# Performance work log

Hardware: AMD Instinct MI355X
Metric: run time of the kernel (lower is better)

## Reference

```python
import jax, jax.numpy as jnp
import numpy as np
from jax import lax

# ---- quantum-kernel constants: flipped model f = Tr[rho(theta) O(patch)] ----
# rho(theta) = (I + sum_i theta_i P_i)/4 over the 15 non-identity 2-qubit Paulis.
# O(patch)  = (M + M^T)/2 where M is the 3x3 patch zero-padded to 16 and reshaped 4x4.
# Both are linear in their inputs, so precompute A[i,k] = Re Tr[P_i O(e_k)] and
# t0[k] = Tr[O(e_k)] once on the host.

def _pauli_features():
    I = np.eye(2, dtype=np.complex64)
    X = np.array([[0, 1], [1, 0]], np.complex64)
    Y = np.array([[0, -1j], [1j, 0]], np.complex64)
    Z = np.array([[1, 0], [0, -1]], np.complex64)
    singles = [I, X, Y, Z]
    paulis = [np.kron(a, b) for a in singles for b in singles][1:]  # 15 non-identity
    A = np.zeros((15, 9), np.float32)
    t0 = np.zeros((9,), np.float32)
    for k in range(9):
        M = np.zeros((4, 4), np.complex64)
        M.flat[k] = 1.0
        O = (M + M.conj().T) / 2.0
        t0[k] = float(np.real(np.trace(O)))
        for i, P in enumerate(paulis):
            A[i, k] = float(np.real(np.trace(P @ O)))
    return A, t0

_A_NP, _T0_NP = _pauli_features()
STRIDE = 1
PAD = (1, 1)  # (pad_h, pad_w)


def setup_inputs() -> dict:
    key = jax.random.key(0)
    k1, k2, k3 = jax.random.split(key, 3)
    x = jax.random.normal(k1, (32, 16, 128, 128), dtype=jnp.float32)
    weight = jax.random.normal(k2, (64, 16, 15), dtype=jnp.float32)
    bias = jax.random.normal(k3, (64, 1), dtype=jnp.float32)
    return {"x": x, "weight": weight, "bias": bias}


def reference(x, weight, bias):
    B, C, H, W = x.shape
    ph, pw = PAD
    Ho = (H - 3 + 2 * ph) // STRIDE + 1
    Wo = (W - 3 + 2 * pw) // STRIDE + 1
    # im2col: [B, C*9, Ho, Wo], channel-major (C slowest, 3x3 row-major fastest)
    patches = lax.conv_general_dilated_patches(
        x, (3, 3), (STRIDE, STRIDE), ((ph, ph), (pw, pw)))
    patches = patches.reshape(B, C, 9, Ho * Wo)  # [B, C, 9, P]

    A = jnp.asarray(_A_NP)    # [15, 9]
    t0 = jnp.asarray(_T0_NP)  # [9]

    # identity part of rho: sum over in-channels of Tr[O]/4 (weight-independent)
    base = jnp.einsum('k,bckp->bp', t0, patches)            # [B, P]
    # Pauli features Tr[P_i O(patch)] per (channel, patch)
    qf = jnp.einsum('ik,bckp->bcip', A, patches)            # [B, C, 15, P]
    out = (base[:, None, :] + jnp.einsum('oci,bcip->bop', weight, qf)) * 0.25
    out = out + bias                                        # bias [O,1] -> [B,O,P]
    return out.reshape(B, weight.shape[0], Ho, Wo)
```

## Files before the change

kernel.cpp:

```cpp
#include <hip/hip_runtime.h>
#include <hip/hip_bf16.h>


typedef short bf16x8 __attribute__((ext_vector_type(8)));
typedef float f32x4 __attribute__((ext_vector_type(4)));

__device__ __forceinline__ void pauli_entry(int s, int r, int c, float& re, float& im) {
    re = 0.f; im = 0.f;
    if (s == 0)      { if (r == c) re = 1.f; }
    else if (s == 1) { if (r != c) re = 1.f; }
    else if (s == 2) { if (r == 0 && c == 1) im = -1.f; else if (r == 1 && c == 0) im = 1.f; }
    else             { if (r == c) re = (r == 0) ? 1.f : -1.f; }
}

__device__ __forceinline__ float A_entry(int i, int k) {
    int j = i + 1, sa = j >> 2, sb = j & 3;
    int r = k >> 2, c = k & 3;
    float ar, ai, br, bi;
    pauli_entry(sa, r >> 1, c >> 1, ar, ai);
    pauli_entry(sb, r & 1, c & 1, br, bi);
    float re1 = ar * br - ai * bi;
    pauli_entry(sa, c >> 1, r >> 1, ar, ai);
    pauli_entry(sb, c & 1, r & 1, br, bi);
    float re2 = ar * br - ai * bi;
    return 0.5f * (re1 + re2);
}

__device__ __forceinline__ short f2bf(float f) {
    union { float f; unsigned int u; } a; a.f = f;
    unsigned int r = a.u + 0x7fffu + ((a.u >> 16) & 1u);
    return (short)(r >> 16);
}

__device__ __forceinline__ unsigned pk_bf16(float a, float b) {
#if __has_builtin(__builtin_amdgcn_cvt_pk_bf16_f32)
    typedef __bf16 bf2 __attribute__((ext_vector_type(2)));
    bf2 r = __builtin_amdgcn_cvt_pk_bf16_f32(a, b);
    union { bf2 v; unsigned u; } cv; cv.v = r;
    return cv.u;
#else
    union { float f; unsigned u; } x, y; x.f = a; y.f = b;
    unsigned ra = x.u + 0x7fffu + ((x.u >> 16) & 1u);
    unsigned rb = y.u + 0x7fffu + ((y.u >> 16) & 1u);
    return (ra >> 16) | (rb & 0xffff0000u);
#endif
}

__global__ __launch_bounds__(256) void prep_kernel(const float* __restrict__ weight,
                                                   short* __restrict__ bfrag) {
    int t = blockIdx.x * 256 + threadIdx.x;
    if (t >= 1280) return;
    int lane  = t & 63;
    int ot    = (t >> 6) & 3;
    int chunk = t >> 8;
    int q     = lane >> 4;
    int o     = ot * 16 + (lane & 15);
    short vals[8];
    #pragma unroll
    for (int j = 0; j < 8; ++j) {
        int gk = chunk * 32 + q * 8 + j;
        float v = 0.f;
        if (gk < 144) {
            int tap = gk >> 4;
            int c   = gk & 15;
            float acc = (tap == 0 || tap == 5) ? 1.f : 0.f;
            const float* w = weight + (o * 16 + c) * 15;
            #pragma unroll
            for (int i = 0; i < 15; ++i) acc += w[i] * A_entry(i, tap);
            v = 0.25f * acc;
        }
        vals[j] = f2bf(v);
    }
    *(bf16x8*)(bfrag + t * 8) = *(bf16x8*)vals;
}

__global__ __launch_bounds__(256) void conv_mfma(const float* __restrict__ x,
                                                 const short* __restrict__ bfrag,
                                                 const float* __restrict__ bias,
                                                 float* __restrict__ out) {
    __shared__ short sx[10 * 136 * 16];

    const int tid  = threadIdx.x;
    const int h0   = blockIdx.x * 8;
    const int b    = blockIdx.y;
    const int lane = tid & 63;
    const int wave = tid >> 6;
    const int q    = lane >> 4;
    const int nlo  = lane & 15;

    const float* xb = x + (size_t)b * 16 * 128 * 128;
    #pragma unroll
    for (int it = 0; it < 11; ++it) {
        int pos = tid + it * 256;
        if (pos < 2720) {
            int seg = pos / 136;
            int w   = pos - seg * 136;
            int row = seg >> 1, chalf = seg & 1;
            int hp  = h0 - 1 + row;
            int xw  = w - 4;
            bool ok = ((unsigned)hp < 128u) && ((unsigned)xw < 128u);
            const float* src = xb + (size_t)(chalf * 8) * 16384 + hp * 128 + xw;
            float v[8];
            #pragma unroll
            for (int j = 0; j < 8; ++j)
                v[j] = ok ? src[(size_t)j * 16384] : 0.f;
            int slot = (chalf ^ (w >> 2)) & 1;
            unsigned* dst = (unsigned*)sx + (row * 136 + w) * 8 + slot * 4;
            #pragma unroll
            for (int j2 = 0; j2 < 4; ++j2)
                dst[j2] = pk_bf16(v[2 * j2], v[2 * j2 + 1]);
        }
    }

    bf16x8 Breg[20];
    #pragma unroll
    for (int i = 0; i < 20; ++i)
        Breg[i] = *(const bf16x8*)(bfrag + (i * 64 + lane) * 8);
    float bv[4];
    #pragma unroll
    for (int ot = 0; ot < 4; ++ot) bv[ot] = bias[ot * 16 + nlo];

    int baseA[5];
    #pragma unroll
    for (int ch = 0; ch < 5; ++ch) {
        int tap = ch * 2 + (q >> 1);
        if (tap > 8) tap = 8;
        int kh = tap / 3, kw = tap - 3 * kh;
        int chalf = q & 1;
        int row0  = wave * 2 + kh;
        int w0    = nlo + kw + 3;
        int slot  = (chalf ^ (w0 >> 2)) & 1;
        baseA[ch] = (row0 * 136 + w0) * 16 + slot * 8;
    }
    __syncthreads();

    #pragma unroll
    for (int rs = 0; rs < 2; ++rs) {
        const int h = h0 + wave * 2 + rs;
        #pragma unroll
        for (int np = 0; np < 4; ++np) {
            f32x4 acc[2][4];
            #pragma unroll
            for (int ot = 0; ot < 4; ++ot) {
                f32x4 ini = { bv[ot], bv[ot], bv[ot], bv[ot] };
                acc[0][ot] = ini;
                acc[1][ot] = ini;
            }
            #pragma unroll
            for (int ch = 0; ch < 5; ++ch) {
                const short* pA = sx + baseA[ch] + rs * 2176 + np * 512;
                bf16x8 A0 = *(const bf16x8*)(pA);
                bf16x8 A1 = *(const bf16x8*)(pA + 256);
                #pragma unroll
                for (int ot = 0; ot < 4; ++ot) {
                    acc[0][ot] = __builtin_amdgcn_mfma_f32_16x16x32_bf16(A0, Breg[ch * 4 + ot], acc[0][ot], 0, 0, 0);
                    acc[1][ot] = __builtin_amdgcn_mfma_f32_16x16x32_bf16(A1, Breg[ch * 4 + ot], acc[1][ot], 0, 0, 0);
                }
            }
            #pragma unroll
            for (int ot = 0; ot < 4; ++ot) {
                float* dst = out + (((size_t)b * 64 + ot * 16 + nlo) * 128 + h) * 128
                           + np * 32 + q * 4;
                *(f32x4*)dst        = acc[0][ot];
                *(f32x4*)(dst + 16) = acc[1][ot];
            }
        }
    }
}

extern "C" void kernel_launch(void* const* d_in, const int* in_sizes, int n_in,
                              void* d_out, int out_size, void* d_ws, size_t ws_size,
                              hipStream_t stream) {
    const float* x      = (const float*)d_in[0];
    const float* weight = (const float*)d_in[1];
    const float* bias   = (const float*)d_in[2];
    float* out   = (float*)d_out;
    short* bfrag = (short*)d_ws;

    prep_kernel<<<5, 256, 0, stream>>>(weight, bfrag);
    dim3 grid(16, 32);
    conv_mfma<<<grid, 256, 0, stream>>>(x, bfrag, bias, out);
}
```

Baseline: 169.4 us.

## Stage MFMA outputs through swizzled LDS for coalesced nontemporal stores

Each wave now keeps the accumulators for a whole output row (all four column chunks) and writes them into a per-wave, XOR-swizzled 32 KB shared buffer. It then reads them back so that each lane stores a contiguous 16-byte piece of a 512-byte output row, using nontemporal stores. The row mapping changes so that each wave handles rows wave and wave+4 rather than two adjacent rows, and the kernel gains a launch_bounds occupancy hint of 2 blocks. The prep kernel also caches the Pauli coefficient table in shared memory. The trade-off is much higher LDS and register use per block, which could limit occupancy.

Measured after the change: 196.1 us. 1.16x slower.

```diff
diff --git a/kernel.cpp b/kernel.cpp
--- a/kernel.cpp
+++ b/kernel.cpp
@@ -48,7 +48,12 @@
 
 __global__ __launch_bounds__(256) void prep_kernel(const float* __restrict__ weight,
                                                    short* __restrict__ bfrag) {
-    int t = blockIdx.x * 256 + threadIdx.x;
+    __shared__ float Ash[135];
+    int tid = threadIdx.x;
+    if (tid < 135) Ash[tid] = A_entry(tid / 9, tid % 9);
+    __syncthreads();
+
+    int t = blockIdx.x * 256 + tid;
     if (t >= 1280) return;
     int lane  = t & 63;
     int ot    = (t >> 6) & 3;
@@ -66,7 +71,7 @@
             float acc = (tap == 0 || tap == 5) ? 1.f : 0.f;
             const float* w = weight + (o * 16 + c) * 15;
             #pragma unroll
-            for (int i = 0; i < 15; ++i) acc += w[i] * A_entry(i, tap);
+            for (int i = 0; i < 15; ++i) acc += w[i] * Ash[i * 9 + tap];
             v = 0.25f * acc;
         }
         vals[j] = f2bf(v);
@@ -74,11 +79,12 @@
     *(bf16x8*)(bfrag + t * 8) = *(bf16x8*)vals;
 }
 
-__global__ __launch_bounds__(256) void conv_mfma(const float* __restrict__ x,
-                                                 const short* __restrict__ bfrag,
-                                                 const float* __restrict__ bias,
-                                                 float* __restrict__ out) {
+__global__ __launch_bounds__(256, 2) void conv_mfma(const float* __restrict__ x,
+                                                    const short* __restrict__ bfrag,
+                                                    const float* __restrict__ bias,
+                                                    float* __restrict__ out) {
     __shared__ short sx[10 * 136 * 16];
+    __shared__ __align__(16) float obuf[8192];
 
     const int tid  = threadIdx.x;
     const int h0   = blockIdx.x * 8;
@@ -127,7 +133,7 @@
         if (tap > 8) tap = 8;
         int kh = tap / 3, kw = tap - 3 * kh;
         int chalf = q & 1;
-        int row0  = wave * 2 + kh;
+        int row0  = wave + kh;
         int w0    = nlo + kw + 3;
         int slot  = (chalf ^ (w0 >> 2)) & 1;
         baseA[ch] = (row0 * 136 + w0) * 16 + slot * 8;
@@ -136,33 +142,49 @@
 
     #pragma unroll
     for (int rs = 0; rs < 2; ++rs) {
-        const int h = h0 + wave * 2 + rs;
+        f32x4 acc[4][4][2];
+        #pragma unroll
+        for (int np = 0; np < 4; ++np)
+            #pragma unroll
+            for (int ot = 0; ot < 4; ++ot) {
+                f32x4 ini = { bv[ot], bv[ot], bv[ot], bv[ot] };
+                acc[np][ot][0] = ini;
+                acc[np][ot][1] = ini;
+            }
         #pragma unroll
         for (int np = 0; np < 4; ++np) {
-            f32x4 acc[2][4];
-            #pragma unroll
-            for (int ot = 0; ot < 4; ++ot) {
-                f32x4 ini = { bv[ot], bv[ot], bv[ot], bv[ot] };
-                acc[0][ot] = ini;
-                acc[1][ot] = ini;
-            }
             #pragma unroll
             for (int ch = 0; ch < 5; ++ch) {
-                const short* pA = sx + baseA[ch] + rs * 2176 + np * 512;
+                const short* pA = sx + baseA[ch] + rs * 8704 + np * 512;
                 bf16x8 A0 = *(const bf16x8*)(pA);
                 bf16x8 A1 = *(const bf16x8*)(pA + 256);
                 #pragma unroll
                 for (int ot = 0; ot < 4; ++ot) {
-                    acc[0][ot] = __builtin_amdgcn_mfma_f32_16x16x32_bf16(A0, Breg[ch * 4 + ot], acc[0][ot], 0, 0, 0);
-                    acc[1][ot] = __builtin_amdgcn_mfma_f32_16x16x32_bf16(A1, Breg[ch * 4 + ot], acc[1][ot], 0, 0, 0);
+                    acc[np][ot][0] = __builtin_amdgcn_mfma_f32_16x16x32_bf16(A0, Breg[ch * 4 + ot], acc[np][ot][0], 0, 0, 0);
+                    acc[np][ot][1] = __builtin_amdgcn_mfma_f32_16x16x32_bf16(A1, Breg[ch * 4 + ot], acc[np][ot][1], 0, 0, 0);
                 }
             }
-            #pragma unroll
-            for (int ot = 0; ot < 4; ++ot) {
-                float* dst = out + (((size_t)b * 64 + ot * 16 + nlo) * 128 + h) * 128
-                           + np * 32 + q * 4;
-                *(f32x4*)dst        = acc[0][ot];
-                *(f32x4*)(dst + 16) = acc[1][ot];
+        }
+        #pragma unroll
+        for (int ot = 0; ot < 4; ++ot) {
+            #pragma unroll
+            for (int np = 0; np < 4; ++np)
+                #pragma unroll
+                for (int mt = 0; mt < 2; ++mt) {
+                    int wpart = np * 32 + mt * 16 + q * 4;
+                    int widx  = wave * 2048 + nlo * 128 + (wpart ^ ((nlo & 7) << 2));
+                    *(f32x4*)(obuf + widx) = acc[np][ot][mt];
+                }
+            float* outp = out + ((((size_t)b * 64 + ot * 16) * 128)
+                                 + h0 + rs * 4 + wave) * 128;
+            #pragma unroll
+            for (int r = 0; r < 8; ++r) {
+                int L  = r * 256 + lane * 4;
+                int o  = (L >> 7) & 15;
+                int wp = L & 127;
+                int ridx = wave * 2048 + o * 128 + (wp ^ ((o & 7) << 2));
+                f32x4 v = *(const f32x4*)(obuf + ridx);
+                __builtin_nontemporal_store(v, (f32x4*)(outp + (size_t)o * 16384 + wp));
             }
         }
     }
```
